# Kernel tuning notes

Measured on AMD Instinct MI355X. Metric: run time of the kernel, lower is better.

## Reference

```python
import jax, jax.numpy as jnp
import numpy as np

N = 100000      # nodes
E = 1600000     # edges (avg degree 16)
F_IN = 15       # num_features from source
H1, H2, OUT = 64, 32, 2
BN_EPS = 1e-5


def _lin(key, out_dim, in_dim):
    return (jax.random.normal(key, (out_dim, in_dim), dtype=jnp.float32)
            * np.float32(1.0 / np.sqrt(in_dim)))


def setup_inputs() -> dict:
    key = jax.random.key(0)
    ks = jax.random.split(key, 16)
    x = jax.random.normal(ks[0], (N, F_IN), dtype=jnp.float32)
    edge_index = jax.random.randint(ks[1], (2, E), 0, N)
    return {
        "x": x,
        "edge_index": edge_index,
        # SAGEConv layer 1 (lin_l on aggregated neighbors w/ bias, lin_r on root no bias)
        "W1l": _lin(ks[2], H1, F_IN), "b1l": jnp.zeros((H1,), jnp.float32),
        "W1r": _lin(ks[3], H1, F_IN),
        "g1": jnp.ones((H1,), jnp.float32), "beta1": jnp.zeros((H1,), jnp.float32),
        # SAGEConv layer 2
        "W2l": _lin(ks[4], H2, H1), "b2l": jnp.zeros((H2,), jnp.float32),
        "W2r": _lin(ks[5], H2, H1),
        "g2": jnp.ones((H2,), jnp.float32), "beta2": jnp.zeros((H2,), jnp.float32),
        # SAGEConv layer 3
        "W3l": _lin(ks[6], OUT, H2), "b3l": jnp.zeros((OUT,), jnp.float32),
        "W3r": _lin(ks[7], OUT, H2),
    }


def sage_conv(x, src, dst, Wl, bl, Wr, n):
    # mean-aggregate neighbor features x[src] at dst, then linear + root linear
    msg = x[src]                                           # [E, d]
    agg = jax.ops.segment_sum(msg, dst, num_segments=n)    # [N, d]
    deg = jax.ops.segment_sum(jnp.ones((src.shape[0],), x.dtype), dst,
                              num_segments=n)              # [N]
    mean = agg / jnp.maximum(deg, 1.0)[:, None]
    return mean @ Wl.T + bl + x @ Wr.T


def batch_norm(x, gamma, beta):
    mu = x.mean(axis=0)
    var = x.var(axis=0)  # biased, as torch BN uses for normalization
    return (x - mu) * jax.lax.rsqrt(var + BN_EPS) * gamma + beta


def reference(x, edge_index, W1l, b1l, W1r, g1, beta1,
              W2l, b2l, W2r, g2, beta2, W3l, b3l, W3r):
    src, dst = edge_index[0], edge_index[1]
    n = x.shape[0]
    h = sage_conv(x, src, dst, W1l, b1l, W1r, n)
    h = jax.nn.relu(batch_norm(h, g1, beta1))
    h = sage_conv(h, src, dst, W2l, b2l, W2r, n)
    h = jax.nn.relu(batch_norm(h, g2, beta2))
    h = sage_conv(h, src, dst, W3l, b3l, W3r, n)
    return jax.nn.log_softmax(h, axis=1)
```

## Files before the change

kernel.cpp:

```cpp
#include <hip/hip_runtime.h>
#include <hip/hip_bf16.h>
#include <math.h>

#define N_NODES 100000
#define N_EDGES 1600000
#define F_IN 15
#define H1 64
#define H2 32
#define BN_EPS 1e-5f
#define NBLK 2048
#define RELU1(v) fmaxf(fmaf((v), scale, shift), 0.f)

__device__ __forceinline__ unsigned short f2bf(float f) {
    unsigned u = __float_as_uint(f);
    u += 0x7FFFu + ((u >> 16) & 1u);
    return (unsigned short)(u >> 16);
}
__device__ __forceinline__ float bf2f(unsigned short h) {
    return __uint_as_float(((unsigned)h) << 16);
}


__global__ void k_deg(const int* __restrict__ dst, int* __restrict__ deg) {
    int e = blockIdx.x * blockDim.x + threadIdx.x;
    if (e < N_EDGES) atomicAdd(&deg[dst[e]], 1);
}

__global__ void k_scan_a(const int* __restrict__ deg, int* __restrict__ off,
                         int* __restrict__ part) {
    __shared__ int s[1024];
    int i = blockIdx.x * 1024 + threadIdx.x;
    int v = (i < N_NODES) ? deg[i] : 0;
    s[threadIdx.x] = v;
    __syncthreads();
    for (int o = 1; o < 1024; o <<= 1) {
        int t = (threadIdx.x >= o) ? s[threadIdx.x - o] : 0;
        __syncthreads();
        s[threadIdx.x] += t;
        __syncthreads();
    }
    if (i < N_NODES) off[i] = s[threadIdx.x] - v;
    if (threadIdx.x == 1023) part[blockIdx.x] = s[1023];
}

__global__ void k_scan_b(int* __restrict__ part, int nb) {
    __shared__ int s[128];
    int v = (threadIdx.x < nb) ? part[threadIdx.x] : 0;
    s[threadIdx.x] = v;
    __syncthreads();
    for (int o = 1; o < 128; o <<= 1) {
        int t = (threadIdx.x >= o) ? s[threadIdx.x - o] : 0;
        __syncthreads();
        s[threadIdx.x] += t;
        __syncthreads();
    }
    if (threadIdx.x < nb) part[threadIdx.x] = s[threadIdx.x] - v;
}

__global__ void k_scan_c(int* __restrict__ off, int* __restrict__ cur,
                         const int* __restrict__ part) {
    int i = blockIdx.x * blockDim.x + threadIdx.x;
    if (i < N_NODES) {
        int v = off[i] + part[i >> 10];
        off[i] = v;
        cur[i] = v;
    }
    if (i == 0) off[N_NODES] = N_EDGES;
}

__global__ void k_fill(const int* __restrict__ src, const int* __restrict__ dst,
                       int* __restrict__ cur, int* __restrict__ srt) {
    int e = blockIdx.x * blockDim.x + threadIdx.x;
    if (e < N_EDGES) {
        int p = atomicAdd(&cur[dst[e]], 1);
        srt[p] = src[e];
    }
}


__launch_bounds__(256)
__global__ void k_l1(const float* __restrict__ x, const int* __restrict__ off,
                     const int* __restrict__ srt,
                     const float* __restrict__ W1l, const float* __restrict__ b1l,
                     const float* __restrict__ W1r,
                     unsigned short* __restrict__ h1b, float* __restrict__ stats) {
    __shared__ float m_lds[4][16], o_lds[4][16];
    __shared__ float sred[2 * H1];
    int lane = threadIdx.x & 63;
    int w = threadIdx.x >> 6;
    int gw = blockIdx.x * 4 + w;
    const int NW = NBLK * 4;

    float wl[F_IN], wr[F_IN];
#pragma unroll
    for (int k = 0; k < F_IN; ++k) {
        wl[k] = W1l[lane * F_IN + k];
        wr[k] = W1r[lane * F_IN + k];
    }
    float bj = b1l[lane];

    if (threadIdx.x < 2 * H1) sred[threadIdx.x] = 0.f;
    __syncthreads();

    float sS = 0.f, sQ = 0.f;
    for (int n = gw; n < N_NODES; n += NW) {
        int o0 = off[n], o1 = off[n + 1];
        float sum = 0.f;
        int i = o0;
        for (; i + 16 <= o1; i += 16) {
            int my = (lane < 16) ? srt[i + lane] : 0;
            float v[16];
#pragma unroll
            for (int b = 0; b < 16; ++b) {
                int s = __shfl(my, b, 64);
                v[b] = (lane < F_IN) ? x[(long)s * F_IN + lane] : 0.f;
            }
#pragma unroll
            for (int b = 0; b < 16; ++b) sum += v[b];
        }
        for (; i + 8 <= o1; i += 8) {
            int my = (lane < 8) ? srt[i + lane] : 0;
            float v[8];
#pragma unroll
            for (int b = 0; b < 8; ++b) {
                int s = __shfl(my, b, 64);
                v[b] = (lane < F_IN) ? x[(long)s * F_IN + lane] : 0.f;
            }
#pragma unroll
            for (int b = 0; b < 8; ++b) sum += v[b];
        }
        for (; i < o1; ++i) {
            int s = srt[i];
            if (lane < F_IN) sum += x[(long)s * F_IN + lane];
        }
        float inv = 1.f / (float)max(o1 - o0, 1);
        if (lane < F_IN) {
            m_lds[w][lane] = sum * inv;
            o_lds[w][lane] = x[(long)n * F_IN + lane];
        }
        float acc = bj;
#pragma unroll
        for (int k = 0; k < F_IN; ++k)
            acc += m_lds[w][k] * wl[k] + o_lds[w][k] * wr[k];
        h1b[(long)n * H1 + lane] = f2bf(acc);
        sS += acc; sQ += acc * acc;
    }
    atomicAdd(&sred[lane], sS);
    atomicAdd(&sred[H1 + lane], sQ);
    __syncthreads();
    if (threadIdx.x < 2 * H1) atomicAdd(&stats[threadIdx.x], sred[threadIdx.x]);
}


__launch_bounds__(256)
__global__ void k_l2(const unsigned short* __restrict__ h1b, const int* __restrict__ off,
                     const int* __restrict__ srt,
                     const float* __restrict__ W2l, const float* __restrict__ b2l,
                     const float* __restrict__ W2r,
                     const float* __restrict__ g1, const float* __restrict__ beta1,
                     const float* __restrict__ stats1,
                     unsigned short* __restrict__ h2b, float* __restrict__ stats2) {
    __shared__ float wlds[H1][H1 + 1];
    __shared__ float meanb[4][H1], ownb[4][H1];
    __shared__ float sred[2 * H2];
    int lane = threadIdx.x & 63;
    int w = threadIdx.x >> 6;
    int gw = blockIdx.x * 4 + w;
    const int NW = NBLK * 4;

    float mu = stats1[lane] * (1.f / N_NODES);
    float var = stats1[H1 + lane] * (1.f / N_NODES) - mu * mu;
    float scale = rsqrtf(var + BN_EPS) * g1[lane];
    float shift = beta1[lane] - mu * scale;

    for (int idx = threadIdx.x; idx < H1 * H1; idx += 256) {
        int jj = idx >> 6, kk = idx & 63;
        wlds[jj][kk] = (jj < H2) ? W2l[jj * H1 + kk] : W2r[(jj - H2) * H1 + kk];
    }
    float bj = (lane < H2) ? b2l[lane] : 0.f;
    if (threadIdx.x < 2 * H2) sred[threadIdx.x] = 0.f;
    __syncthreads();

    float sS = 0.f, sQ = 0.f;
    for (int n = gw; n < N_NODES; n += NW) {
        int o0 = off[n], o1 = off[n + 1];
        float sum = 0.f;
        int i = o0;
        for (; i + 16 <= o1; i += 16) {
            int my = (lane < 16) ? srt[i + lane] : 0;
            float v[16];
#pragma unroll
            for (int b = 0; b < 16; ++b) {
                int s = __shfl(my, b, 64);
                v[b] = bf2f(h1b[(long)s * H1 + lane]);
            }
#pragma unroll
            for (int b = 0; b < 16; ++b) sum += RELU1(v[b]);
        }
        for (; i + 8 <= o1; i += 8) {
            int my = (lane < 8) ? srt[i + lane] : 0;
            float v[8];
#pragma unroll
            for (int b = 0; b < 8; ++b) {
                int s = __shfl(my, b, 64);
                v[b] = bf2f(h1b[(long)s * H1 + lane]);
            }
#pragma unroll
            for (int b = 0; b < 8; ++b) sum += RELU1(v[b]);
        }
        for (; i < o1; ++i) {
            int s = srt[i];
            sum += RELU1(bf2f(h1b[(long)s * H1 + lane]));
        }
        float inv = 1.f / (float)max(o1 - o0, 1);
        meanb[w][lane] = sum * inv;
        ownb[w][lane] = RELU1(bf2f(h1b[(long)n * H1 + lane]));

        const float* bsel = (lane < H2) ? &meanb[w][0] : &ownb[w][0];
        float acc = bj;
#pragma unroll
        for (int k = 0; k < H1; ++k) acc += bsel[k] * wlds[lane][k];
        float other = __shfl_xor(acc, 32, 64);
        if (lane < H2) {
            float hp = acc + other;
            h2b[(long)n * H2 + lane] = f2bf(hp);
            sS += hp; sQ += hp * hp;
        }
    }
    if (lane < H2) {
        atomicAdd(&sred[lane], sS);
        atomicAdd(&sred[H2 + lane], sQ);
    }
    __syncthreads();
    if (threadIdx.x < 2 * H2) atomicAdd(&stats2[threadIdx.x], sred[threadIdx.x]);
}


__launch_bounds__(256)
__global__ void k_l3(const unsigned short* __restrict__ h2b, const int* __restrict__ off,
                     const int* __restrict__ srt,
                     const float* __restrict__ W3l, const float* __restrict__ b3l,
                     const float* __restrict__ W3r,
                     const float* __restrict__ g2, const float* __restrict__ beta2,
                     const float* __restrict__ stats2, float* __restrict__ out) {
    int lane = threadIdx.x & 63;
    int w = threadIdx.x >> 6;
    int h = lane >> 5;
    int j = lane & 31;
    int gw = blockIdx.x * 4 + w;
    const int NW = NBLK * 4;

    float mu = stats2[j] * (1.f / N_NODES);
    float var = stats2[H2 + j] * (1.f / N_NODES) - mu * mu;
    float scale = rsqrtf(var + BN_EPS) * g2[j];
    float shift = beta2[j] - mu * scale;

    float wl0 = W3l[j], wl1 = W3l[H2 + j];
    float wr0 = W3r[j], wr1 = W3r[H2 + j];
    float b0 = b3l[0], b1 = b3l[1];

    for (int p = gw; p < N_NODES / 2; p += NW) {
        int n = p * 2 + h;
        int o0 = off[n], o1 = off[n + 1];
        float sum = 0.f;
        int i = o0;
        for (; i + 16 <= o1; i += 16) {
            int sidx[16];
#pragma unroll
            for (int b = 0; b < 16; ++b) sidx[b] = srt[i + b];
            float v[16];
#pragma unroll
            for (int b = 0; b < 16; ++b) v[b] = bf2f(h2b[(long)sidx[b] * H2 + j]);
#pragma unroll
            for (int b = 0; b < 16; ++b) sum += RELU1(v[b]);
        }
        for (; i + 8 <= o1; i += 8) {
            int sidx[8];
#pragma unroll
            for (int b = 0; b < 8; ++b) sidx[b] = srt[i + b];
            float v[8];
#pragma unroll
            for (int b = 0; b < 8; ++b) v[b] = bf2f(h2b[(long)sidx[b] * H2 + j]);
#pragma unroll
            for (int b = 0; b < 8; ++b) sum += RELU1(v[b]);
        }
        for (; i < o1; ++i) {
            int s = srt[i];
            sum += RELU1(bf2f(h2b[(long)s * H2 + j]));
        }
        float inv = 1.f / (float)max(o1 - o0, 1);
        float meanj = sum * inv;
        float ownj = RELU1(bf2f(h2b[(long)n * H2 + j]));
        float p0 = meanj * wl0 + ownj * wr0;
        float p1 = meanj * wl1 + ownj * wr1;
#pragma unroll
        for (int s = 16; s > 0; s >>= 1) {
            p0 += __shfl_xor(p0, s, 32);
            p1 += __shfl_xor(p1, s, 32);
        }
        if (j == 0) {
            float z0 = p0 + b0, z1 = p1 + b1;
            float m = fmaxf(z0, z1);
            float l = m + logf(__expf(z0 - m) + __expf(z1 - m));
            out[(long)n * 2 + 0] = z0 - l;
            out[(long)n * 2 + 1] = z1 - l;
        }
    }
}


extern "C" void kernel_launch(void* const* d_in, const int* in_sizes, int n_in,
                              void* d_out, int out_size, void* d_ws, size_t ws_size,
                              hipStream_t stream) {
    const float* x    = (const float*)d_in[0];
    const int*   ei   = (const int*)d_in[1];
    const float* W1l  = (const float*)d_in[2];
    const float* b1l  = (const float*)d_in[3];
    const float* W1r  = (const float*)d_in[4];
    const float* g1   = (const float*)d_in[5];
    const float* bt1  = (const float*)d_in[6];
    const float* W2l  = (const float*)d_in[7];
    const float* b2l  = (const float*)d_in[8];
    const float* W2r  = (const float*)d_in[9];
    const float* g2   = (const float*)d_in[10];
    const float* bt2  = (const float*)d_in[11];
    const float* W3l  = (const float*)d_in[12];
    const float* b3l  = (const float*)d_in[13];
    const float* W3r  = (const float*)d_in[14];
    float* out = (float*)d_out;

    float* stats1 = (float*)d_ws;
    float* stats2 = stats1 + 128;
    int* deg  = (int*)d_ws + 256;
    int* off  = deg + 100096;
    int* cur  = off + 100096;
    int* srt  = cur + 100096;
    int* part = srt + 1600000;
    unsigned short* h1b = (unsigned short*)(part + 256);
    unsigned short* h2b = h1b + (size_t)N_NODES * H1;

    const int* srcv = ei;
    const int* dstv = ei + N_EDGES;

    hipMemsetAsync(d_ws, 0, (256 + 100096) * sizeof(int), stream);

    k_deg   <<<(N_EDGES + 255) / 256, 256, 0, stream>>>(dstv, deg);
    k_scan_a<<<98, 1024, 0, stream>>>(deg, off, part);
    k_scan_b<<<1, 128, 0, stream>>>(part, 98);
    k_scan_c<<<(N_NODES + 255) / 256, 256, 0, stream>>>(off, cur, part);
    k_fill  <<<(N_EDGES + 255) / 256, 256, 0, stream>>>(srcv, dstv, cur, srt);
    k_l1    <<<NBLK, 256, 0, stream>>>(x, off, srt, W1l, b1l, W1r, h1b, stats1);
    k_l2    <<<NBLK, 256, 0, stream>>>(h1b, off, srt, W2l, b2l, W2r, g1, bt1, stats1, h2b, stats2);
    k_l3    <<<NBLK, 256, 0, stream>>>(h2b, off, srt, W3l, b3l, W3r, g2, bt2, stats2, out);
}
```

Measured before the change: 637.8 us.

## Transform before aggregating in layers 2 and 3 and pack layer-1 gathers

Layers 2 and 3 now apply the linear weights per node first and then mean-aggregate the projected features. This works because the mean and the linear map commute. The neighbor gather in layer 2 shrinks from 64 bf16 values to 32 per edge, and in layer 3 from 32 to 2 floats per edge, processed one node per thread. Layer 1 now packs four edges per wave load, using 16-lane groups followed by a shuffle reduction. The cost is extra kernel launches and intermediate buffers (t2b, r2, h2p, t3, r3) written to and read from global memory.

New measurement: 588.3 us. 7.8% less time.

```diff
diff --git a/kernel.cpp b/kernel.cpp
--- a/kernel.cpp
+++ b/kernel.cpp
@@ -18,6 +18,9 @@
 }
 __device__ __forceinline__ float bf2f(unsigned short h) {
     return __uint_as_float(((unsigned)h) << 16);
+}
+__device__ __forceinline__ float bcast(float v, int k) {
+    return __int_as_float(__builtin_amdgcn_readlane(__float_as_int(v), k));
 }
 
 
@@ -87,15 +90,17 @@
     __shared__ float m_lds[4][16], o_lds[4][16];
     __shared__ float sred[2 * H1];
     int lane = threadIdx.x & 63;
+    int h4 = lane >> 4;
+    int k  = lane & 15;
     int w = threadIdx.x >> 6;
     int gw = blockIdx.x * 4 + w;
     const int NW = NBLK * 4;
 
     float wl[F_IN], wr[F_IN];
 #pragma unroll
-    for (int k = 0; k < F_IN; ++k) {
-        wl[k] = W1l[lane * F_IN + k];
-        wr[k] = W1r[lane * F_IN + k];
+    for (int kk = 0; kk < F_IN; ++kk) {
+        wl[kk] = W1l[lane * F_IN + kk];
+        wr[kk] = W1r[lane * F_IN + kk];
     }
     float bj = b1l[lane];
 
@@ -109,30 +114,20 @@
         int i = o0;
         for (; i + 16 <= o1; i += 16) {
             int my = (lane < 16) ? srt[i + lane] : 0;
-            float v[16];
-#pragma unroll
-            for (int b = 0; b < 16; ++b) {
-                int s = __shfl(my, b, 64);
-                v[b] = (lane < F_IN) ? x[(long)s * F_IN + lane] : 0.f;
+            float v[4];
+#pragma unroll
+            for (int b = 0; b < 4; ++b) {
+                int s = __shfl(my, b * 4 + h4, 64);
+                v[b] = (k < F_IN) ? x[(long)s * F_IN + k] : 0.f;
             }
-#pragma unroll
-            for (int b = 0; b < 16; ++b) sum += v[b];
-        }
-        for (; i + 8 <= o1; i += 8) {
-            int my = (lane < 8) ? srt[i + lane] : 0;
-            float v[8];
-#pragma unroll
-            for (int b = 0; b < 8; ++b) {
-                int s = __shfl(my, b, 64);
-                v[b] = (lane < F_IN) ? x[(long)s * F_IN + lane] : 0.f;
-            }
-#pragma unroll
-            for (int b = 0; b < 8; ++b) sum += v[b];
+            sum += (v[0] + v[1]) + (v[2] + v[3]);
         }
         for (; i < o1; ++i) {
             int s = srt[i];
             if (lane < F_IN) sum += x[(long)s * F_IN + lane];
         }
+        sum += __shfl_xor(sum, 16, 64);
+        sum += __shfl_xor(sum, 32, 64);
         float inv = 1.f / (float)max(o1 - o0, 1);
         if (lane < F_IN) {
             m_lds[w][lane] = sum * inv;
@@ -140,8 +135,8 @@
         }
         float acc = bj;
 #pragma unroll
-        for (int k = 0; k < F_IN; ++k)
-            acc += m_lds[w][k] * wl[k] + o_lds[w][k] * wr[k];
+        for (int kk = 0; kk < F_IN; ++kk)
+            acc += m_lds[w][kk] * wl[kk] + o_lds[w][kk] * wr[kk];
         h1b[(long)n * H1 + lane] = f2bf(acc);
         sS += acc; sQ += acc * acc;
     }
@@ -152,17 +147,13 @@
 }
 
 
-__launch_bounds__(256)
-__global__ void k_l2(const unsigned short* __restrict__ h1b, const int* __restrict__ off,
-                     const int* __restrict__ srt,
+__launch_bounds__(256, 2)
+__global__ void k_t2(const unsigned short* __restrict__ h1b,
                      const float* __restrict__ W2l, const float* __restrict__ b2l,
                      const float* __restrict__ W2r,
                      const float* __restrict__ g1, const float* __restrict__ beta1,
                      const float* __restrict__ stats1,
-                     unsigned short* __restrict__ h2b, float* __restrict__ stats2) {
-    __shared__ float wlds[H1][H1 + 1];
-    __shared__ float meanb[4][H1], ownb[4][H1];
-    __shared__ float sred[2 * H2];
+                     unsigned short* __restrict__ t2b, float* __restrict__ r2) {
     int lane = threadIdx.x & 63;
     int w = threadIdx.x >> 6;
     int gw = blockIdx.x * 4 + w;
@@ -173,11 +164,36 @@
     float scale = rsqrtf(var + BN_EPS) * g1[lane];
     float shift = beta1[lane] - mu * scale;
 
-    for (int idx = threadIdx.x; idx < H1 * H1; idx += 256) {
-        int jj = idx >> 6, kk = idx & 63;
-        wlds[jj][kk] = (jj < H2) ? W2l[jj * H1 + kk] : W2r[(jj - H2) * H1 + kk];
-    }
-    float bj = (lane < H2) ? b2l[lane] : 0.f;
+    const float* wsrc = (lane < H2) ? (W2l + lane * H1) : (W2r + (lane - H2) * H1);
+    float wreg[H1];
+#pragma unroll
+    for (int kk = 0; kk < H1; ++kk) wreg[kk] = wsrc[kk];
+    float addc = (lane < H2) ? 0.f : b2l[lane - H2];
+
+    for (int n = gw; n < N_NODES; n += NW) {
+        float y = RELU1(bf2f(h1b[(long)n * H1 + lane]));
+        float acc = addc;
+#pragma unroll
+        for (int kk = 0; kk < H1; ++kk)
+            acc = fmaf(bcast(y, kk), wreg[kk], acc);
+        if (lane < H2) t2b[(long)n * H2 + lane] = f2bf(acc);
+        else           r2[(long)n * H2 + (lane - H2)] = acc;
+    }
+}
+
+
+__launch_bounds__(256)
+__global__ void k_a2(const unsigned short* __restrict__ t2b, const float* __restrict__ r2,
+                     const int* __restrict__ off, const int* __restrict__ srt,
+                     float* __restrict__ h2p, float* __restrict__ stats2) {
+    __shared__ float sred[2 * H2];
+    int lane = threadIdx.x & 63;
+    int j = lane & 31;
+    int h = lane >> 5;
+    int w = threadIdx.x >> 6;
+    int gw = blockIdx.x * 4 + w;
+    const int NW = NBLK * 4;
+
     if (threadIdx.x < 2 * H2) sred[threadIdx.x] = 0.f;
     __syncthreads();
 
@@ -188,48 +204,36 @@
         int i = o0;
         for (; i + 16 <= o1; i += 16) {
             int my = (lane < 16) ? srt[i + lane] : 0;
-            float v[16];
-#pragma unroll
-            for (int b = 0; b < 16; ++b) {
-                int s = __shfl(my, b, 64);
-                v[b] = bf2f(h1b[(long)s * H1 + lane]);
+            float v[8];
+#pragma unroll
+            for (int b = 0; b < 8; ++b) {
+                int s0 = __shfl(my, 2 * b, 64);
+                int s1 = __shfl(my, 2 * b + 1, 64);
+                int s = h ? s1 : s0;
+                v[b] = bf2f(t2b[(long)s * H2 + j]);
             }
-#pragma unroll
-            for (int b = 0; b < 16; ++b) sum += RELU1(v[b]);
-        }
-        for (; i + 8 <= o1; i += 8) {
-            int my = (lane < 8) ? srt[i + lane] : 0;
-            float v[8];
-#pragma unroll
-            for (int b = 0; b < 8; ++b) {
-                int s = __shfl(my, b, 64);
-                v[b] = bf2f(h1b[(long)s * H1 + lane]);
-            }
-#pragma unroll
-            for (int b = 0; b < 8; ++b) sum += RELU1(v[b]);
-        }
-        for (; i < o1; ++i) {
+            sum += (((v[0]+v[1])+(v[2]+v[3])) + ((v[4]+v[5])+(v[6]+v[7])));
+        }
+        for (; i + 2 <= o1; i += 2) {
+            int s0 = srt[i], s1 = srt[i + 1];
+            int s = h ? s1 : s0;
+            sum += bf2f(t2b[(long)s * H2 + j]);
+        }
+        if (i < o1) {
             int s = srt[i];
-            sum += RELU1(bf2f(h1b[(long)s * H1 + lane]));
-        }
+            if (!h) sum += bf2f(t2b[(long)s * H2 + j]);
+        }
+        sum += __shfl_xor(sum, 32, 64);
         float inv = 1.f / (float)max(o1 - o0, 1);
-        meanb[w][lane] = sum * inv;
-        ownb[w][lane] = RELU1(bf2f(h1b[(long)n * H1 + lane]));
-
-        const float* bsel = (lane < H2) ? &meanb[w][0] : &ownb[w][0];
-        float acc = bj;
-#pragma unroll
-        for (int k = 0; k < H1; ++k) acc += bsel[k] * wlds[lane][k];
-        float other = __shfl_xor(acc, 32, 64);
         if (lane < H2) {
-            float hp = acc + other;
-            h2b[(long)n * H2 + lane] = f2bf(hp);
+            float hp = fmaf(sum, inv, r2[(long)n * H2 + j]);
+            h2p[(long)n * H2 + j] = hp;
             sS += hp; sQ += hp * hp;
         }
     }
     if (lane < H2) {
-        atomicAdd(&sred[lane], sS);
-        atomicAdd(&sred[H2 + lane], sQ);
+        atomicAdd(&sred[j], sS);
+        atomicAdd(&sred[H2 + j], sQ);
     }
     __syncthreads();
     if (threadIdx.x < 2 * H2) atomicAdd(&stats2[threadIdx.x], sred[threadIdx.x]);
@@ -237,16 +241,16 @@
 
 
 __launch_bounds__(256)
-__global__ void k_l3(const unsigned short* __restrict__ h2b, const int* __restrict__ off,
-                     const int* __restrict__ srt,
+__global__ void k_t3(const float* __restrict__ h2p,
                      const float* __restrict__ W3l, const float* __restrict__ b3l,
                      const float* __restrict__ W3r,
                      const float* __restrict__ g2, const float* __restrict__ beta2,
-                     const float* __restrict__ stats2, float* __restrict__ out) {
+                     const float* __restrict__ stats2,
+                     float* __restrict__ t3, float* __restrict__ r3) {
     int lane = threadIdx.x & 63;
+    int j = lane & 31;
+    int h = lane >> 5;
     int w = threadIdx.x >> 6;
-    int h = lane >> 5;
-    int j = lane & 31;
     int gw = blockIdx.x * 4 + w;
     const int NW = NBLK * 4;
 
@@ -261,51 +265,54 @@
 
     for (int p = gw; p < N_NODES / 2; p += NW) {
         int n = p * 2 + h;
-        int o0 = off[n], o1 = off[n + 1];
-        float sum = 0.f;
-        int i = o0;
-        for (; i + 16 <= o1; i += 16) {
-            int sidx[16];
-#pragma unroll
-            for (int b = 0; b < 16; ++b) sidx[b] = srt[i + b];
-            float v[16];
-#pragma unroll
-            for (int b = 0; b < 16; ++b) v[b] = bf2f(h2b[(long)sidx[b] * H2 + j]);
-#pragma unroll
-            for (int b = 0; b < 16; ++b) sum += RELU1(v[b]);
-        }
-        for (; i + 8 <= o1; i += 8) {
-            int sidx[8];
-#pragma unroll
-            for (int b = 0; b < 8; ++b) sidx[b] = srt[i + b];
-            float v[8];
-#pragma unroll
-            for (int b = 0; b < 8; ++b) v[b] = bf2f(h2b[(long)sidx[b] * H2 + j]);
-#pragma unroll
-            for (int b = 0; b < 8; ++b) sum += RELU1(v[b]);
-        }
-        for (; i < o1; ++i) {
-            int s = srt[i];
-            sum += RELU1(bf2f(h2b[(long)s * H2 + j]));
-        }
-        float inv = 1.f / (float)max(o1 - o0, 1);
-        float meanj = sum * inv;
-        float ownj = RELU1(bf2f(h2b[(long)n * H2 + j]));
-        float p0 = meanj * wl0 + ownj * wr0;
-        float p1 = meanj * wl1 + ownj * wr1;
+        float y = RELU1(h2p[(long)n * H2 + j]);
+        float p0 = y * wl0, p1 = y * wl1, q0 = y * wr0, q1 = y * wr1;
 #pragma unroll
         for (int s = 16; s > 0; s >>= 1) {
             p0 += __shfl_xor(p0, s, 32);
             p1 += __shfl_xor(p1, s, 32);
+            q0 += __shfl_xor(q0, s, 32);
+            q1 += __shfl_xor(q1, s, 32);
         }
         if (j == 0) {
-            float z0 = p0 + b0, z1 = p1 + b1;
-            float m = fmaxf(z0, z1);
-            float l = m + logf(__expf(z0 - m) + __expf(z1 - m));
-            out[(long)n * 2 + 0] = z0 - l;
-            out[(long)n * 2 + 1] = z1 - l;
-        }
-    }
+            *(float2*)(t3 + (long)n * 2) = make_float2(p0, p1);
+            *(float2*)(r3 + (long)n * 2) = make_float2(q0 + b0, q1 + b1);
+        }
+    }
+}
+
+
+__launch_bounds__(256)
+__global__ void k_a3(const float* __restrict__ t3, const float* __restrict__ r3,
+                     const int* __restrict__ off, const int* __restrict__ srt,
+                     float* __restrict__ out) {
+    int n = blockIdx.x * 256 + threadIdx.x;
+    if (n >= N_NODES) return;
+    int o0 = off[n], o1 = off[n + 1];
+    float s0 = 0.f, s1 = 0.f;
+    int i = o0;
+    for (; i + 8 <= o1; i += 8) {
+        int sidx[8];
+#pragma unroll
+        for (int b = 0; b < 8; ++b) sidx[b] = srt[i + b];
+        float2 v[8];
+#pragma unroll
+        for (int b = 0; b < 8; ++b) v[b] = *(const float2*)(t3 + (long)sidx[b] * 2);
+#pragma unroll
+        for (int b = 0; b < 8; ++b) { s0 += v[b].x; s1 += v[b].y; }
+    }
+    for (; i < o1; ++i) {
+        float2 v = *(const float2*)(t3 + (long)srt[i] * 2);
+        s0 += v.x; s1 += v.y;
+    }
+    float inv = 1.f / (float)max(o1 - o0, 1);
+    float2 rr = *(const float2*)(r3 + (long)n * 2);
+    float z0 = fmaf(s0, inv, rr.x);
+    float z1 = fmaf(s1, inv, rr.y);
+    float m = fmaxf(z0, z1);
+    float l = m + logf(__expf(z0 - m) + __expf(z1 - m));
+    out[(long)n * 2 + 0] = z0 - l;
+    out[(long)n * 2 + 1] = z1 - l;
 }
 
 
@@ -337,7 +344,11 @@
     int* srt  = cur + 100096;
     int* part = srt + 1600000;
     unsigned short* h1b = (unsigned short*)(part + 256);
-    unsigned short* h2b = h1b + (size_t)N_NODES * H1;
+    float* h2p = (float*)h1b;
+    unsigned short* t2b = (unsigned short*)((int*)(part + 256) + 3200000);
+    float* r2 = (float*)((int*)(part + 256) + 3200000 + 1600000);
+    float* t3 = r2 + 3200000;
+    float* r3 = t3 + 200000;
 
     const int* srcv = ei;
     const int* dstv = ei + N_EDGES;
@@ -350,6 +361,8 @@
     k_scan_c<<<(N_NODES + 255) / 256, 256, 0, stream>>>(off, cur, part);
     k_fill  <<<(N_EDGES + 255) / 256, 256, 0, stream>>>(srcv, dstv, cur, srt);
     k_l1    <<<NBLK, 256, 0, stream>>>(x, off, srt, W1l, b1l, W1r, h1b, stats1);
-    k_l2    <<<NBLK, 256, 0, stream>>>(h1b, off, srt, W2l, b2l, W2r, g1, bt1, stats1, h2b, stats2);
-    k_l3    <<<NBLK, 256, 0, stream>>>(h2b, off, srt, W3l, b3l, W3r, g2, bt2, stats2, out);
-}
+    k_t2    <<<NBLK, 256, 0, stream>>>(h1b, W2l, b2l, W2r, g1, bt1, stats1, t2b, r2);
+    k_a2    <<<NBLK, 256, 0, stream>>>(t2b, r2, off, srt, h2p, stats2);
+    k_t3    <<<NBLK, 256, 0, stream>>>(h2p, W3l, b3l, W3r, g2, bt2, stats2, t3, r3);
+    k_a3    <<<(N_NODES + 255) / 256, 256, 0, stream>>>(t3, r3, off, srt, out);
+}
```
